# Kernel tuning notes

Measured on AMD Instinct MI355X. Metric: run time of the kernel, lower is better.

## Reference

```python
import jax, jax.numpy as jnp
import numpy as np

QMAX = 127.0  # 2**(bits-1) - 1 for bits=8, signed symmetric


def _quantize_signed_symmetric(t):
    # per-tensor symmetric: scale = max|t| / qmax, q = clamp(round(t/scale))
    scale = jnp.max(jnp.abs(t)) / QMAX
    q = jnp.clip(jnp.round(t / scale), -QMAX, QMAX)
    return q, scale


def setup_inputs() -> dict:
    key = jax.random.key(0)
    k1, k2, k3 = jax.random.split(key, 3)
    N, D_IN, D_OUT = 16384, 1024, 1024
    x = jax.random.normal(k1, (N, D_IN), dtype=jnp.float32)
    weight = jax.random.normal(k2, (D_OUT, D_IN), dtype=jnp.float32) * 0.02
    bias = jax.random.normal(k3, (D_OUT,), dtype=jnp.float32) * 0.01
    return {"x": x, "weight": weight, "bias": bias}


def reference(x, weight, bias):
    # weight quantization (cached in torch; recomputed here, same math)
    qw, w_scale = _quantize_signed_symmetric(weight)
    qw_t = qw.astype(jnp.int32).T            # [D_IN, D_OUT]
    # activation quantization
    qx, x_scale = _quantize_signed_symmetric(x)
    qx = qx.astype(jnp.int32)                # [N, D_IN]
    # int32 matmul, then per-tensor dequant + bias
    acc = qx @ qw_t                          # int32 [N, D_OUT]
    y = acc.astype(jnp.float32) * (x_scale * w_scale)
    return y + bias
```

## Files before the change

kernel.cpp:

```cpp
#include <hip/hip_runtime.h>

#define QMAX 127.0f

typedef int int4v __attribute__((ext_vector_type(4)));
typedef float float4v __attribute__((ext_vector_type(4)));

__device__ __forceinline__ float amax4(float4 v) {
    return fmaxf(fmaxf(fabsf(v.x), fabsf(v.y)), fmaxf(fabsf(v.z), fabsf(v.w)));
}
__device__ __forceinline__ int qone(float v, float s) {
    float q = fminf(fmaxf(rintf(v / s), -QMAX), QMAX);
    return (int)q;
}
__device__ __forceinline__ int qpack4(float4 v, float s) {
    return (qone(v.x, s) & 255) | ((qone(v.y, s) & 255) << 8) |
           ((qone(v.z, s) & 255) << 16) | ((qone(v.w, s) & 255) << 24);
}

__global__ void absmax2_kernel(const float4* __restrict__ px, int n4x,
                               const float4* __restrict__ pw, int n4w,
                               int gx, int* __restrict__ amax) {
    const float4* p; int n4; int* out; int nb, bid;
    if ((int)blockIdx.x < gx) { p = px; n4 = n4x; out = amax + 0; nb = gx; bid = blockIdx.x; }
    else { p = pw; n4 = n4w; out = amax + 1; nb = gridDim.x - gx; bid = blockIdx.x - gx; }
    const int S = nb * blockDim.x;
    int i = bid * blockDim.x + threadIdx.x;
    float a = 0.f, b = 0.f, c = 0.f, d = 0.f;
    for (; i + 3 * S < n4; i += 4 * S) {
        float4 v0 = p[i];
        float4 v1 = p[i + S];
        float4 v2 = p[i + 2 * S];
        float4 v3 = p[i + 3 * S];
        a = fmaxf(a, amax4(v0));
        b = fmaxf(b, amax4(v1));
        c = fmaxf(c, amax4(v2));
        d = fmaxf(d, amax4(v3));
    }
    for (; i < n4; i += S) a = fmaxf(a, amax4(p[i]));
    float m = fmaxf(fmaxf(a, b), fmaxf(c, d));
    for (int off = 32; off; off >>= 1) m = fmaxf(m, __shfl_down(m, off, 64));
    __shared__ float sm[4];
    if ((threadIdx.x & 63) == 0) sm[threadIdx.x >> 6] = m;
    __syncthreads();
    if (threadIdx.x == 0) {
        float bm = fmaxf(fmaxf(sm[0], sm[1]), fmaxf(sm[2], sm[3]));
        atomicMax(out, (int)__float_as_uint(bm));
    }
}

__global__ void quantw_kernel(const float4* __restrict__ sw, int4v* __restrict__ dw,
                              int n16w, int kshift, int KC,
                              const int* __restrict__ amax) {
    const float scale = __uint_as_float((unsigned)amax[1]) / QMAX;
    const int stride = gridDim.x * blockDim.x;
    for (int i = blockIdx.x * blockDim.x + threadIdx.x; i < n16w; i += stride) {
        float4 v0 = sw[4 * i + 0];
        float4 v1 = sw[4 * i + 1];
        float4 v2 = sw[4 * i + 2];
        float4 v3 = sw[4 * i + 3];
        int4v o = { qpack4(v0, scale), qpack4(v1, scale),
                    qpack4(v2, scale), qpack4(v3, scale) };
        const int n = i >> kshift;
        const int kg = i & ((1 << kshift) - 1);
        const int kc = kg >> 2, q = kg & 3;
        const int g = n >> 4, r = n & 15;
        dw[(g * KC + kc) * 64 + q * 16 + r] = o;
    }
}

__global__ __launch_bounds__(1024, 4) void gemm_i8_kernel(
        const float* __restrict__ x, const char* __restrict__ qb,
        const float4* __restrict__ bias4, const int* __restrict__ amax,
        float* __restrict__ out, int M, int N, int K) {
    extern __shared__ char sA[];

    const int KC = K >> 6;
    const int CH = KC >> 2;
    const int tid = threadIdx.x;
    const int lane = tid & 63;
    const int wv = tid >> 6;
    const int m0 = blockIdx.x * 64;

    const int si = wv >> 2;
    const int skcl = wv & 3;
    const int srow = m0 + si * 16 + (lane & 15);
    const int sk0 = skcl * 64 + (lane >> 4) * 16;
    const float* sbase = x + (size_t)srow * K + sk0;
    const int sslot = si * 256 + skcl * 64 + lane;

    const float xs = __uint_as_float((unsigned)amax[0]) / QMAX;

    const char* bbase = qb + (size_t)(wv * 4) * KC * 1024 + lane * 16;

#define LOADB(Bb, kc)                                                        \
    do { _Pragma("unroll") for (int j = 0; j < 4; ++j)                       \
        Bb[j] = *(const int4v*)(bbase + ((size_t)j * KC + (kc)) * 1024);     \
    } while (0)
#define LOADA(Af, kcl)                                                       \
    do { _Pragma("unroll") for (int i = 0; i < 4; ++i)                       \
        Af[i] = sAv[i * 256 + (kcl) * 64 + lane];                            \
    } while (0)
#define MF(Bb, Af)                                                           \
    do { _Pragma("unroll") for (int j = 0; j < 4; ++j)                       \
        _Pragma("unroll") for (int i = 0; i < 4; ++i)                        \
            acc[j][i] = __builtin_amdgcn_mfma_i32_16x16x64_i8(               \
                Bb[j], Af[i], acc[j][i], 0, 0, 0);                           \
    } while (0)
#define ISSUEX(h)                                                            \
    do { const float4* sp = (const float4*)(sbase + (h) * 256);              \
        xr0 = sp[0]; xr1 = sp[1]; xr2 = sp[2]; xr3 = sp[3];                  \
    } while (0)
#define QWRITE(h)                                                            \
    do { int4v o = { qpack4(xr0, xs), qpack4(xr1, xs),                       \
                     qpack4(xr2, xs), qpack4(xr3, xs) };                     \
        ((int4v*)(sA + ((h) & 1) * 16384))[sslot] = o;                       \
    } while (0)

    float4 xr0, xr1, xr2, xr3;
    int4v B0[4], B1[4], Af[4];

    ISSUEX(0);
    LOADB(B0, 0);
    QWRITE(0);
    __syncthreads();

    int4v acc[4][4];
    const int4v zero = {0, 0, 0, 0};
#pragma unroll
    for (int j = 0; j < 4; ++j)
#pragma unroll
        for (int i = 0; i < 4; ++i) acc[j][i] = zero;

#pragma unroll 1
    for (int h = 0; h < CH; ++h) {
        const int4v* sAv = (const int4v*)(sA + (h & 1) * 16384);
        const int kc0 = h * 4;
        const bool more = (h + 1 < CH);
        if (more) ISSUEX(h + 1);
        LOADB(B1, kc0 + 1); LOADA(Af, 0); MF(B0, Af);
        LOADB(B0, kc0 + 2); LOADA(Af, 1); MF(B1, Af);
        LOADB(B1, kc0 + 3); LOADA(Af, 2); MF(B0, Af);
        if (more) LOADB(B0, kc0 + 4);
        LOADA(Af, 3); MF(B1, Af);
        if (more) {
            QWRITE(h + 1);
            __syncthreads();
        }
    }

    const float sc = xs * (__uint_as_float((unsigned)amax[1]) / QMAX);
    const int quad = lane >> 4;
    const int rbase = m0 + (lane & 15);
    const int cb4 = wv * 16;
#pragma unroll
    for (int j = 0; j < 4; ++j) {
        const float4 bv = bias4[cb4 + j * 4 + quad];
#pragma unroll
        for (int i = 0; i < 4; ++i) {
            const int row = rbase + i * 16;
            float4v v;
            v[0] = (float)acc[j][i][0] * sc + bv.x;
            v[1] = (float)acc[j][i][1] * sc + bv.y;
            v[2] = (float)acc[j][i][2] * sc + bv.z;
            v[3] = (float)acc[j][i][3] * sc + bv.w;
            *((float4v*)(out + (size_t)row * N) + cb4 + j * 4 + quad) = v;
        }
    }
}

extern "C" void kernel_launch(void* const* d_in, const int* in_sizes, int n_in,
                              void* d_out, int out_size, void* d_ws, size_t ws_size,
                              hipStream_t stream) {
    const float* x = (const float*)d_in[0];
    const float* w = (const float*)d_in[1];
    const float* bias = (const float*)d_in[2];
    float* out = (float*)d_out;

    const int xn = in_sizes[0];
    const int wn = in_sizes[1];
    const int N = in_sizes[2];
    const int K = wn / N;
    const int M = xn / K;
    const int KC = K >> 6;
    const int kshift = __builtin_ctz(K >> 4);

    int* amax = (int*)d_ws;
    char* qw = (char*)d_ws + 1024;

    const int GAX = 2048, GAW = 256;
    absmax2_kernel<<<GAX + GAW, 256, 0, stream>>>(
        (const float4*)x, xn / 4, (const float4*)w, wn / 4, GAX, amax);

    quantw_kernel<<<256, 256, 0, stream>>>(
        (const float4*)w, (int4v*)qw, wn / 16, kshift, KC, amax);

    gemm_i8_kernel<<<M / 64, 1024, 32768, stream>>>(
        x, qw, (const float4*)bias, amax, out, M, N, K);
}
```

Measured before the change: 191.2 us.

## Split activation prefetch into halves and interleave LDS loads with MFMA groups

The GEMM main loop now loads the next activation chunk in two halves. It quantizes the first half mid-iteration to cut the float4 registers held across the MFMA block from four to two. LDS A-fragment loads are narrowed from four to two per step and interleaved with the MFMAs. The last iteration is peeled so the conditional 'more' branches disappear. The aim is lower register pressure under the 1024-thread launch bounds and better overlap of memory with matrix ops, at the cost of a reordered B-load schedule that may expose different latencies.

```diff
diff --git a/kernel.cpp b/kernel.cpp
--- a/kernel.cpp
+++ b/kernel.cpp
@@ -85,7 +85,7 @@
     const int skcl = wv & 3;
     const int srow = m0 + si * 16 + (lane & 15);
     const int sk0 = skcl * 64 + (lane >> 4) * 16;
-    const float* sbase = x + (size_t)srow * K + sk0;
+    const float4* sbase4 = (const float4*)(x + (size_t)srow * K + sk0);
     const int sslot = si * 256 + skcl * 64 + lane;
 
     const float xs = __uint_as_float((unsigned)amax[0]) / QMAX;
@@ -96,32 +96,35 @@
     do { _Pragma("unroll") for (int j = 0; j < 4; ++j)                       \
         Bb[j] = *(const int4v*)(bbase + ((size_t)j * KC + (kc)) * 1024);     \
     } while (0)
-#define LOADA(Af, kcl)                                                       \
-    do { _Pragma("unroll") for (int i = 0; i < 4; ++i)                       \
-        Af[i] = sAv[i * 256 + (kcl) * 64 + lane];                            \
-    } while (0)
-#define MF(Bb, Af)                                                           \
+#define LOADA2(kcl, ih)                                                      \
+    do { _Pragma("unroll") for (int i = 0; i < 2; ++i)                       \
+        Af[i] = sAv[((ih) * 2 + i) * 256 + (kcl) * 64 + lane];               \
+    } while (0)
+#define MF2(Bb, ih)                                                          \
     do { _Pragma("unroll") for (int j = 0; j < 4; ++j)                       \
-        _Pragma("unroll") for (int i = 0; i < 4; ++i)                        \
-            acc[j][i] = __builtin_amdgcn_mfma_i32_16x16x64_i8(               \
-                Bb[j], Af[i], acc[j][i], 0, 0, 0);                           \
-    } while (0)
-#define ISSUEX(h)                                                            \
-    do { const float4* sp = (const float4*)(sbase + (h) * 256);              \
-        xr0 = sp[0]; xr1 = sp[1]; xr2 = sp[2]; xr3 = sp[3];                  \
-    } while (0)
-#define QWRITE(h)                                                            \
-    do { int4v o = { qpack4(xr0, xs), qpack4(xr1, xs),                       \
-                     qpack4(xr2, xs), qpack4(xr3, xs) };                     \
-        ((int4v*)(sA + ((h) & 1) * 16384))[sslot] = o;                       \
-    } while (0)
-
-    float4 xr0, xr1, xr2, xr3;
-    int4v B0[4], B1[4], Af[4];
-
-    ISSUEX(0);
+        _Pragma("unroll") for (int i = 0; i < 2; ++i)                        \
+            acc[j][(ih) * 2 + i] = __builtin_amdgcn_mfma_i32_16x16x64_i8(    \
+                Bb[j], Af[i], acc[j][(ih) * 2 + i], 0, 0, 0);                \
+    } while (0)
+#define KCQUAD(Bb0, Bb1, kcl0, kcl1)                                         \
+    do { LOADA2(kcl0, 0); MF2(Bb0, 0); LOADA2(kcl0, 1); MF2(Bb0, 1);         \
+         LOADA2(kcl1, 0); MF2(Bb1, 0); LOADA2(kcl1, 1); MF2(Bb1, 1);         \
+    } while (0)
+#define ISSUEA(h) do { xr0 = sbase4[(h) * 64]; xr1 = sbase4[(h) * 64 + 1]; } while (0)
+#define ISSUEB(h) do { xr0 = sbase4[(h) * 64 + 2]; xr1 = sbase4[(h) * 64 + 3]; } while (0)
+
+    float4 xr0, xr1;
+    int qa0, qa1;
+    int4v B0[4], B1[4], Af[2];
+
+    ISSUEA(0);
     LOADB(B0, 0);
-    QWRITE(0);
+    qa0 = qpack4(xr0, xs); qa1 = qpack4(xr1, xs);
+    ISSUEB(0);
+    {
+        int4v o = { qa0, qa1, qpack4(xr0, xs), qpack4(xr1, xs) };
+        ((int4v*)sA)[sslot] = o;
+    }
     __syncthreads();
 
     int4v acc[4][4];
@@ -132,20 +135,32 @@
         for (int i = 0; i < 4; ++i) acc[j][i] = zero;
 
 #pragma unroll 1
-    for (int h = 0; h < CH; ++h) {
+    for (int h = 0; h < CH - 1; ++h) {
         const int4v* sAv = (const int4v*)(sA + (h & 1) * 16384);
         const int kc0 = h * 4;
-        const bool more = (h + 1 < CH);
-        if (more) ISSUEX(h + 1);
-        LOADB(B1, kc0 + 1); LOADA(Af, 0); MF(B0, Af);
-        LOADB(B0, kc0 + 2); LOADA(Af, 1); MF(B1, Af);
-        LOADB(B1, kc0 + 3); LOADA(Af, 2); MF(B0, Af);
-        if (more) LOADB(B0, kc0 + 4);
-        LOADA(Af, 3); MF(B1, Af);
-        if (more) {
-            QWRITE(h + 1);
-            __syncthreads();
+        ISSUEA(h + 1);
+        LOADB(B1, kc0 + 1);
+        KCQUAD(B0, B1, 0, 1);
+        LOADB(B0, kc0 + 2);
+        qa0 = qpack4(xr0, xs); qa1 = qpack4(xr1, xs);
+        ISSUEB(h + 1);
+        LOADB(B1, kc0 + 3);
+        KCQUAD(B0, B1, 2, 3);
+        LOADB(B0, kc0 + 4);
+        {
+            int4v o = { qa0, qa1, qpack4(xr0, xs), qpack4(xr1, xs) };
+            ((int4v*)(sA + ((h + 1) & 1) * 16384))[sslot] = o;
         }
+        __syncthreads();
+    }
+    {
+        const int4v* sAv = (const int4v*)(sA + ((CH - 1) & 1) * 16384);
+        const int kc0 = (CH - 1) * 4;
+        LOADB(B1, kc0 + 1);
+        KCQUAD(B0, B1, 0, 1);
+        LOADB(B0, kc0 + 2);
+        LOADB(B1, kc0 + 3);
+        KCQUAD(B0, B1, 2, 3);
     }
 
     const float sc = xs * (__uint_as_float((unsigned)amax[1]) / QMAX);
```

Result: no change. 190.2 us (-0.5%).
